# Optimization experiments

Measured on AMD Instinct MI355X. Metric: run time of the kernel, lower is better.

Reference implementation:

```python
import jax, jax.numpy as jnp
import numpy as np

B, S, D = 2, 2048, 1024
DFF = 2048
E_FFN = 8
E_ZERO = 4
E_TOT = E_FFN + E_ZERO
TOP_K = 2


def setup_inputs() -> dict:
    key = jax.random.key(0)
    k1, k2, k3, k4 = jax.random.split(key, 4)
    x = jax.random.normal(k1, (B, S, D), dtype=jnp.float32)
    gate_w = jax.random.normal(k2, (E_TOT, D), dtype=jnp.float32) * (1.0 / np.sqrt(D))
    expert_bias = jnp.zeros((E_TOT,), dtype=jnp.float32)
    w1 = jax.random.normal(k3, (E_FFN, DFF, D), dtype=jnp.float32) * (1.0 / np.sqrt(D))
    w2 = jax.random.normal(k4, (E_FFN, D, DFF), dtype=jnp.float32) * (1.0 / np.sqrt(DFF))
    return {"x": x, "gate_w": gate_w, "expert_bias": expert_bias, "w1": w1, "w2": w2}


def reference(x, gate_w, expert_bias, w1, w2):
    # Router: logits over all (FFN + zero) experts, plus adaptive bias buffer.
    logits = jnp.einsum('btd,ed->bte', x, gate_w) + expert_bias  # [B,S,E_TOT]
    topk_logits, topk_idx = jax.lax.top_k(logits, TOP_K)          # [B,S,K]
    topk_w = jax.nn.softmax(topk_logits, axis=-1)                 # renorm over top-k
    # Dense per-token per-expert combine weight (each expert appears at most once in top-k).
    onehot = jax.nn.one_hot(topk_idx, E_TOT, dtype=x.dtype)       # [B,S,K,E_TOT]
    w = jnp.einsum('btk,btke->bte', topk_w, onehot)               # [B,S,E_TOT]
    w_ffn = w[..., :E_FFN]                                        # [B,S,E_FFN]
    w_zero = jnp.sum(w[..., E_FFN:], axis=-1)                     # [B,S] (zero experts = identity)
    # Dense grouped FFN over all experts (eval mode: dropout is identity).
    h = jax.nn.silu(jnp.einsum('btd,efd->btef', x, w1))           # [B,S,E,DFF]
    y = jnp.einsum('btef,edf->bted', h, w2)                       # [B,S,E,D]
    out = jnp.einsum('bte,bted->btd', w_ffn, y) + w_zero[..., None] * x
    return out
```

## Files before the change

kernel.cpp:

```cpp
#include <hip/hip_runtime.h>
#include <math.h>

#define NTOK   4096
#define DMODEL 1024
#define DFFN   2048
#define NEXP   8
#define ETOT   12
#define MAXA   8192
#define WL1MAX (MAXA / 128 + NEXP)
#define WL2MAX (MAXA / 128 + NEXP)

typedef short  bf16x8 __attribute__((ext_vector_type(8)));
typedef float  f32x4  __attribute__((ext_vector_type(4)));

__device__ __forceinline__ unsigned short f2bf(float f) {
  unsigned int u = __float_as_uint(f);
  unsigned int r = (u + 0x7fffu + ((u >> 16) & 1u)) >> 16;
  return (unsigned short)r;
}

#define G2L16(g, l)                                                        \
  __builtin_amdgcn_global_load_lds(                                        \
      (const __attribute__((address_space(1))) void*)(g),                  \
      (__attribute__((address_space(3))) void*)(l), 16, 0, 0)

__global__ void cvt_kernel(const float* __restrict__ in,
                           unsigned short* __restrict__ outp, int n8) {
  int i = blockIdx.x * blockDim.x + threadIdx.x;
  if (i >= n8) return;
  const float4* p = (const float4*)in;
  float4 v0 = p[2 * (size_t)i], v1 = p[2 * (size_t)i + 1];
  ushort4 u0, u1;
  u0.x = f2bf(v0.x); u0.y = f2bf(v0.y); u0.z = f2bf(v0.z); u0.w = f2bf(v0.w);
  u1.x = f2bf(v1.x); u1.y = f2bf(v1.y); u1.z = f2bf(v1.z); u1.w = f2bf(v1.w);
  ((ushort4*)outp)[2 * (size_t)i]     = u0;
  ((ushort4*)outp)[2 * (size_t)i + 1] = u1;
}

__launch_bounds__(256)
__global__ void logits_kernel(const float* __restrict__ x,
                              const float* __restrict__ gw,
                              const float* __restrict__ eb,
                              float* __restrict__ logits) {
  __shared__ float gws[ETOT * DMODEL];
  int tid = threadIdx.x;
  const float4* gw4 = (const float4*)gw;
  float4* gws4 = (float4*)gws;
  #pragma unroll
  for (int i = 0; i < (ETOT * DMODEL / 4) / 256; i++)
    gws4[tid + i * 256] = gw4[tid + i * 256];
  __syncthreads();

  int sub = tid >> 4;
  int l16 = tid & 15;
  int tok = blockIdx.x * 16 + sub;
  const float4* xr = (const float4*)(x + (size_t)tok * DMODEL);

  float s[ETOT] = {};
  #pragma unroll
  for (int j = 0; j < 16; j++) {
    float4 xv = xr[l16 + j * 16];
    #pragma unroll
    for (int e = 0; e < ETOT; e++) {
      float4 g = gws4[e * (DMODEL / 4) + l16 + j * 16];
      s[e] += xv.x * g.x + xv.y * g.y + xv.z * g.z + xv.w * g.w;
    }
  }
  #pragma unroll
  for (int e = 0; e < ETOT; e++) {
    #pragma unroll
    for (int m = 8; m >= 1; m >>= 1) s[e] += __shfl_xor(s[e], m, 64);
  }
  if (l16 == 0) {
    #pragma unroll
    for (int e = 0; e < ETOT; e++)
      logits[(size_t)tok * ETOT + e] = s[e] + eb[e];
  }
}

__global__ void topk_kernel(const float* __restrict__ logits,
                            int* __restrict__ cnt,
                            int* __restrict__ choice,
                            float* __restrict__ chw,
                            float* __restrict__ wz) {
  int t = blockIdx.x * blockDim.x + threadIdx.x;
  if (t >= NTOK) return;
  const float4* lr = (const float4*)(logits + (size_t)t * ETOT);
  float4 a = lr[0], b = lr[1], c = lr[2];
  float lg[ETOT] = { a.x, a.y, a.z, a.w, b.x, b.y, b.z, b.w, c.x, c.y, c.z, c.w };
  int i1 = 0; float m1 = lg[0];
  #pragma unroll
  for (int e = 1; e < ETOT; e++) if (lg[e] > m1) { m1 = lg[e]; i1 = e; }
  int i2 = -1; float m2 = -3.4e38f;
  #pragma unroll
  for (int e = 0; e < ETOT; e++) { if (e == i1) continue; if (lg[e] > m2) { m2 = lg[e]; i2 = e; } }
  float ex = expf(m2 - m1);
  float w0 = 1.f / (1.f + ex);
  float w1 = ex / (1.f + ex);
  int ee[2] = { i1, i2 };
  float ww[2] = { w0, w1 };
  float z = 0.f;
  #pragma unroll
  for (int k = 0; k < 2; k++) {
    choice[t * 2 + k] = ee[k];
    chw[t * 2 + k]    = ww[k];
    if (ee[k] < NEXP) atomicAdd(&cnt[ee[k]], 1);
    else              z += ww[k];
  }
  wz[t] = z;
}

__global__ void scan_kernel(const int* __restrict__ cnt,
                            int* __restrict__ offs,
                            int* __restrict__ cursor,
                            int* __restrict__ wl1, int* __restrict__ nw1,
                            int* __restrict__ wl2, int* __restrict__ nw2) {
  if (threadIdx.x == 0) {
    int a = 0;
    for (int e = 0; e < NEXP; e++) { offs[e] = a; cursor[e] = a; a += cnt[e]; }
    int n1 = 0, n2 = 0;
    for (int e = 0; e < NEXP; e++) {
      int c = cnt[e];
      for (int mb = 0; mb * 128 < c; mb++) wl1[n1++] = e | (mb << 8);
      for (int mb = 0; mb * 128 < c; mb++) wl2[n2++] = e | (mb << 8);
    }
    *nw1 = n1; *nw2 = n2;
  }
}

__global__ void assign_kernel(const int* __restrict__ choice,
                              int* __restrict__ cursor,
                              int* __restrict__ a_row,
                              int* __restrict__ tok_list) {
  int t = blockIdx.x * blockDim.x + threadIdx.x;
  if (t >= NTOK) return;
  #pragma unroll
  for (int k = 0; k < 2; k++) {
    int e = choice[2 * t + k];
    if (e < NEXP) {
      int pos = atomicAdd(&cursor[e], 1);
      a_row[2 * t + k] = pos;
      tok_list[pos] = t;
    } else {
      a_row[2 * t + k] = -1;
    }
  }
}

template <int BM, int NDIM, int KDIM, bool SILU, bool AGATHER>
__launch_bounds__(256)
__global__ void ffn_gemm(const unsigned short* __restrict__ Abf,
                         const unsigned short* __restrict__ Bw,
                         const int* __restrict__ cnt,
                         const int* __restrict__ offs,
                         const int* __restrict__ tok_list,
                         const int* __restrict__ wl,
                         const int* __restrict__ nwork,
                         unsigned short* __restrict__ OutBf,
                         float* __restrict__ OutF) {
  constexpr int NB = NDIM / 128;
  constexpr int MI = BM / 32;
  constexpr int AJ = BM / 64;
  int id = blockIdx.x;
  int nb = id & (NB - 1);
  int wb = id / NB;
  if (wb >= *nwork) return;
  int w  = wl[wb];
  int e  = w & 255;
  int mb = w >> 8;
  int count = cnt[e];
  int m0 = mb * BM;
  int off = offs[e];
  int n0 = nb * 128;
  const unsigned short* B = Bw + (size_t)e * NDIM * KDIM;

  __shared__ unsigned short lA[2][BM * 32];
  __shared__ unsigned short lB[2][128 * 32];

  int tid  = threadIdx.x;
  int lane = tid & 63;
  int wv = tid >> 6;
  int wm = wv >> 1, wn = wv & 1;
  int lr = lane & 15, lk8 = (lane >> 4) * 8;

  int srow = tid >> 2;
  int scol = (tid & 3) * 8;
  const unsigned short* aSrc[AJ];
  const unsigned short* bSrc[2];
  #pragma unroll
  for (int j = 0; j < AJ; j++) {
    int rr = m0 + j * 64 + srow;
    if (rr >= count) rr = count - 1;
    if (AGATHER) aSrc[j] = Abf + (size_t)tok_list[off + rr] * KDIM + scol;
    else         aSrc[j] = Abf + (size_t)(off + rr) * KDIM + scol;
  }
  #pragma unroll
  for (int j = 0; j < 2; j++)
    bSrc[j] = B + (size_t)(n0 + j * 64 + srow) * KDIM + scol;

  f32x4 acc[MI][4] = {};

#define STAGE(b, kk)                                                        \
  do {                                                                      \
    int kb_ = (kk) * 32;                                                    \
    _Pragma("unroll")                                                       \
    for (int j = 0; j < AJ; j++) G2L16(aSrc[j] + kb_, &lA[b][j * 2048 + tid * 8]); \
    _Pragma("unroll")                                                       \
    for (int j = 0; j < 2; j++)  G2L16(bSrc[j] + kb_, &lB[b][j * 2048 + tid * 8]); \
  } while (0)

#define COMPUTE(b)                                                          \
  do {                                                                      \
    bf16x8 af[MI], bq[4];                                                   \
    _Pragma("unroll")                                                       \
    for (int mi = 0; mi < MI; mi++)                                         \
      af[mi] = *(const bf16x8*)&lA[b][(wm * (BM / 2) + mi * 16 + lr) * 32 + lk8]; \
    _Pragma("unroll")                                                       \
    for (int ni = 0; ni < 4; ni++)                                          \
      bq[ni] = *(const bf16x8*)&lB[b][(wn * 64 + ni * 16 + lr) * 32 + lk8]; \
    _Pragma("unroll")                                                       \
    for (int mi = 0; mi < MI; mi++)                                         \
      _Pragma("unroll")                                                     \
      for (int ni = 0; ni < 4; ni++)                                        \
        acc[mi][ni] = __builtin_amdgcn_mfma_f32_16x16x32_bf16(af[mi], bq[ni], acc[mi][ni], 0, 0, 0); \
  } while (0)

  constexpr int NK = KDIM / 32;
  STAGE(0, 0);
  __syncthreads();
  #pragma unroll 1
  for (int kk = 0; kk < NK; kk += 2) {
    if (kk + 1 < NK) STAGE(1, kk + 1);
    COMPUTE(0);
    __syncthreads();
    if (kk + 1 < NK) {
      if (kk + 2 < NK) STAGE(0, kk + 2);
      COMPUTE(1);
      __syncthreads();
    }
  }
#undef STAGE
#undef COMPUTE

  int rb = (lane >> 4) * 4;
  #pragma unroll
  for (int mi = 0; mi < MI; mi++) {
    #pragma unroll
    for (int i = 0; i < 4; i++) {
      int grow = m0 + wm * (BM / 2) + mi * 16 + rb + i;
      if (grow >= count) continue;
      #pragma unroll
      for (int ni = 0; ni < 4; ni++) {
        int gcol = n0 + wn * 64 + ni * 16 + lr;
        float v = acc[mi][ni][i];
        if (SILU) {
          float s = v * __builtin_amdgcn_rcpf(
                        1.f + __builtin_amdgcn_exp2f(-v * 1.44269504088896f));
          OutBf[(size_t)(off + grow) * NDIM + gcol] = f2bf(s);
        } else {
          OutF[(size_t)(off + grow) * NDIM + gcol] = v;
        }
      }
    }
  }
}

__global__ void combine_kernel(const float* __restrict__ x,
                               const float* __restrict__ Y,
                               const int* __restrict__ a_row,
                               const float* __restrict__ chw,
                               const float* __restrict__ wz,
                               float* __restrict__ out) {
  int t = blockIdx.x;
  int d = threadIdx.x * 4;
  const float4 xv = *(const float4*)&x[(size_t)t * DMODEL + d];
  float z = wz[t];
  float4 o; o.x = z * xv.x; o.y = z * xv.y; o.z = z * xv.z; o.w = z * xv.w;
  #pragma unroll
  for (int k = 0; k < 2; k++) {
    int r = a_row[2 * t + k];
    if (r >= 0) {
      float w = chw[2 * t + k];
      const float4 yv = *(const float4*)&Y[(size_t)r * DMODEL + d];
      o.x += w * yv.x; o.y += w * yv.y; o.z += w * yv.z; o.w += w * yv.w;
    }
  }
  *(float4*)&out[(size_t)t * DMODEL + d] = o;
}

extern "C" void kernel_launch(void* const* d_in, const int* in_sizes, int n_in,
                              void* d_out, int out_size, void* d_ws, size_t ws_size,
                              hipStream_t stream) {
  const float* x  = (const float*)d_in[0];
  const float* gw = (const float*)d_in[1];
  const float* eb = (const float*)d_in[2];
  const float* w1 = (const float*)d_in[3];
  const float* w2 = (const float*)d_in[4];
  float* out = (float*)d_out;

  char* ws = (char*)d_ws;
  size_t o = 0;
  int*   cnt     = (int*)(ws + o);  o += 8 * sizeof(int);
  int*   offs    = (int*)(ws + o);  o += 8 * sizeof(int);
  int*   cursor  = (int*)(ws + o);  o += 8 * sizeof(int);
  int*   nw1     = (int*)(ws + o);  o += sizeof(int);
  int*   nw2     = (int*)(ws + o);  o += sizeof(int);
  o = (o + 255) & ~(size_t)255;
  int*   wl1     = (int*)(ws + o);  o += WL1MAX * sizeof(int);
  int*   wl2     = (int*)(ws + o);  o += WL2MAX * sizeof(int);
  o = (o + 255) & ~(size_t)255;
  int*   choice  = (int*)(ws + o);  o += (size_t)2 * NTOK * sizeof(int);
  float* chw     = (float*)(ws + o); o += (size_t)2 * NTOK * sizeof(float);
  float* wzv     = (float*)(ws + o); o += (size_t)NTOK * sizeof(float);
  int*   a_row   = (int*)(ws + o);  o += (size_t)2 * NTOK * sizeof(int);
  int*   tok     = (int*)(ws + o);  o += (size_t)MAXA * sizeof(int);
  float* logits  = (float*)(ws + o); o += (size_t)NTOK * ETOT * sizeof(float);
  o = (o + 255) & ~(size_t)255;
  unsigned short* Xb  = (unsigned short*)(ws + o); o += (size_t)NTOK * DMODEL * sizeof(unsigned short);
  unsigned short* W1b = (unsigned short*)(ws + o); o += (size_t)NEXP * DFFN * DMODEL * sizeof(unsigned short);
  unsigned short* W2b = (unsigned short*)(ws + o); o += (size_t)NEXP * DMODEL * DFFN * sizeof(unsigned short);
  unsigned short* H   = (unsigned short*)(ws + o); o += (size_t)MAXA * DFFN * sizeof(unsigned short);
  float* Y = (float*)W1b;

  hipMemsetAsync(cnt, 0, 8 * sizeof(int), stream);

  cvt_kernel<<<dim3((NEXP * DFFN * DMODEL / 8 + 255) / 256), dim3(256), 0, stream>>>(
      w1, W1b, NEXP * DFFN * DMODEL / 8);
  cvt_kernel<<<dim3((NEXP * DMODEL * DFFN / 8 + 255) / 256), dim3(256), 0, stream>>>(
      w2, W2b, NEXP * DMODEL * DFFN / 8);
  cvt_kernel<<<dim3((NTOK * DMODEL / 8 + 255) / 256), dim3(256), 0, stream>>>(
      x, Xb, NTOK * DMODEL / 8);

  logits_kernel<<<dim3(NTOK / 16), dim3(256), 0, stream>>>(x, gw, eb, logits);
  topk_kernel<<<dim3(NTOK / 256), dim3(256), 0, stream>>>(logits, cnt, choice, chw, wzv);
  scan_kernel<<<dim3(1), dim3(64), 0, stream>>>(cnt, offs, cursor, wl1, nw1, wl2, nw2);
  assign_kernel<<<dim3(NTOK / 256), dim3(256), 0, stream>>>(choice, cursor, a_row, tok);

  ffn_gemm<128, DFFN, DMODEL, true, true>
      <<<dim3(WL1MAX * (DFFN / 128)), dim3(256), 0, stream>>>(
      Xb, W1b, cnt, offs, tok, wl1, nw1, H, nullptr);
  ffn_gemm<128, DMODEL, DFFN, false, false>
      <<<dim3(WL2MAX * (DMODEL / 128)), dim3(256), 0, stream>>>(
      H, W2b, cnt, offs, tok, wl2, nw2, nullptr, Y);

  combine_kernel<<<dim3(NTOK), dim3(256), 0, stream>>>(x, Y, a_row, chw, wzv, out);
}
```

Before: 197.7 us.

## Fuse fp32-to-bf16 weight conversion into grouped FFN GEMM B-tile loads

Removes the two standalone conversion kernels that turned w1 and w2 into bf16 workspace copies. The GEMMs now load fp32 weight tiles into registers, convert them to bf16 and write them to LDS, with the load overlapped against the MFMA compute of the other buffer. This avoids writing and re-reading roughly 64 MB of bf16 weights. In exchange each GEMM block reads twice the weight bytes in fp32, and the same weight tile is re-read and re-converted by every M-block of an expert. Y moves to its own workspace region because it can no longer alias W1b.

```diff
diff --git a/kernel.cpp b/kernel.cpp
--- a/kernel.cpp
+++ b/kernel.cpp
@@ -1,4 +1,5 @@
 #include <hip/hip_runtime.h>
+#include <hip/hip_bf16.h>
 #include <math.h>
 
 #define NTOK   4096
@@ -10,13 +11,19 @@
 #define WL1MAX (MAXA / 128 + NEXP)
 #define WL2MAX (MAXA / 128 + NEXP)
 
-typedef short  bf16x8 __attribute__((ext_vector_type(8)));
-typedef float  f32x4  __attribute__((ext_vector_type(4)));
+typedef short          bf16x8   __attribute__((ext_vector_type(8)));
+typedef float          f32x4    __attribute__((ext_vector_type(4)));
+typedef unsigned short ushort8v __attribute__((ext_vector_type(8)));
 
 __device__ __forceinline__ unsigned short f2bf(float f) {
   unsigned int u = __float_as_uint(f);
   unsigned int r = (u + 0x7fffu + ((u >> 16) & 1u)) >> 16;
   return (unsigned short)r;
+}
+
+__device__ __forceinline__ unsigned short f2bfh(float f) {
+  __hip_bfloat16 h = __float2bfloat16(f);
+  return __builtin_bit_cast(unsigned short, h);
 }
 
 #define G2L16(g, l)                                                        \
@@ -150,7 +157,7 @@
 template <int BM, int NDIM, int KDIM, bool SILU, bool AGATHER>
 __launch_bounds__(256)
 __global__ void ffn_gemm(const unsigned short* __restrict__ Abf,
-                         const unsigned short* __restrict__ Bw,
+                         const float* __restrict__ BwF,
                          const int* __restrict__ cnt,
                          const int* __restrict__ offs,
                          const int* __restrict__ tok_list,
@@ -172,7 +179,7 @@
   int m0 = mb * BM;
   int off = offs[e];
   int n0 = nb * 128;
-  const unsigned short* B = Bw + (size_t)e * NDIM * KDIM;
+  const float* B = BwF + (size_t)e * NDIM * KDIM;
 
   __shared__ unsigned short lA[2][BM * 32];
   __shared__ unsigned short lB[2][128 * 32];
@@ -186,7 +193,7 @@
   int srow = tid >> 2;
   int scol = (tid & 3) * 8;
   const unsigned short* aSrc[AJ];
-  const unsigned short* bSrc[2];
+  const float* bSrc[2];
   #pragma unroll
   for (int j = 0; j < AJ; j++) {
     int rr = m0 + j * 64 + srow;
@@ -199,14 +206,36 @@
     bSrc[j] = B + (size_t)(n0 + j * 64 + srow) * KDIM + scol;
 
   f32x4 acc[MI][4] = {};
-
-#define STAGE(b, kk)                                                        \
+  f32x4 breg[2][2];
+
+#define STAGEA(b, kk)                                                       \
   do {                                                                      \
     int kb_ = (kk) * 32;                                                    \
     _Pragma("unroll")                                                       \
     for (int j = 0; j < AJ; j++) G2L16(aSrc[j] + kb_, &lA[b][j * 2048 + tid * 8]); \
-    _Pragma("unroll")                                                       \
-    for (int j = 0; j < 2; j++)  G2L16(bSrc[j] + kb_, &lB[b][j * 2048 + tid * 8]); \
+  } while (0)
+
+#define LOADB(kk)                                                           \
+  do {                                                                      \
+    int kb_ = (kk) * 32;                                                    \
+    _Pragma("unroll")                                                       \
+    for (int j = 0; j < 2; j++) {                                           \
+      const f32x4* p_ = (const f32x4*)(bSrc[j] + kb_);                      \
+      breg[j][0] = p_[0]; breg[j][1] = p_[1];                               \
+    }                                                                       \
+  } while (0)
+
+#define WRITEB(b)                                                           \
+  do {                                                                      \
+    _Pragma("unroll")                                                       \
+    for (int j = 0; j < 2; j++) {                                           \
+      ushort8v u_;                                                          \
+      u_[0] = f2bfh(breg[j][0][0]); u_[1] = f2bfh(breg[j][0][1]);           \
+      u_[2] = f2bfh(breg[j][0][2]); u_[3] = f2bfh(breg[j][0][3]);           \
+      u_[4] = f2bfh(breg[j][1][0]); u_[5] = f2bfh(breg[j][1][1]);           \
+      u_[6] = f2bfh(breg[j][1][2]); u_[7] = f2bfh(breg[j][1][3]);           \
+      *(ushort8v*)&lB[b][j * 2048 + tid * 8] = u_;                          \
+    }                                                                       \
   } while (0)
 
 #define COMPUTE(b)                                                          \
@@ -226,20 +255,26 @@
   } while (0)
 
   constexpr int NK = KDIM / 32;
-  STAGE(0, 0);
+  LOADB(0);
+  STAGEA(0, 0);
+  WRITEB(0);
   __syncthreads();
   #pragma unroll 1
   for (int kk = 0; kk < NK; kk += 2) {
-    if (kk + 1 < NK) STAGE(1, kk + 1);
+    if (kk + 1 < NK) { LOADB(kk + 1); STAGEA(1, kk + 1); }
     COMPUTE(0);
+    if (kk + 1 < NK) WRITEB(1);
     __syncthreads();
     if (kk + 1 < NK) {
-      if (kk + 2 < NK) STAGE(0, kk + 2);
+      if (kk + 2 < NK) { LOADB(kk + 2); STAGEA(0, kk + 2); }
       COMPUTE(1);
+      if (kk + 2 < NK) WRITEB(0);
       __syncthreads();
     }
   }
-#undef STAGE
+#undef STAGEA
+#undef LOADB
+#undef WRITEB
 #undef COMPUTE
 
   int rb = (lane >> 4) * 4;
@@ -316,18 +351,12 @@
   int*   tok     = (int*)(ws + o);  o += (size_t)MAXA * sizeof(int);
   float* logits  = (float*)(ws + o); o += (size_t)NTOK * ETOT * sizeof(float);
   o = (o + 255) & ~(size_t)255;
-  unsigned short* Xb  = (unsigned short*)(ws + o); o += (size_t)NTOK * DMODEL * sizeof(unsigned short);
-  unsigned short* W1b = (unsigned short*)(ws + o); o += (size_t)NEXP * DFFN * DMODEL * sizeof(unsigned short);
-  unsigned short* W2b = (unsigned short*)(ws + o); o += (size_t)NEXP * DMODEL * DFFN * sizeof(unsigned short);
-  unsigned short* H   = (unsigned short*)(ws + o); o += (size_t)MAXA * DFFN * sizeof(unsigned short);
-  float* Y = (float*)W1b;
+  unsigned short* Xb = (unsigned short*)(ws + o); o += (size_t)NTOK * DMODEL * sizeof(unsigned short);
+  unsigned short* H  = (unsigned short*)(ws + o); o += (size_t)MAXA * DFFN * sizeof(unsigned short);
+  float*          Y  = (float*)(ws + o);          o += (size_t)MAXA * DMODEL * sizeof(float);
 
   hipMemsetAsync(cnt, 0, 8 * sizeof(int), stream);
 
-  cvt_kernel<<<dim3((NEXP * DFFN * DMODEL / 8 + 255) / 256), dim3(256), 0, stream>>>(
-      w1, W1b, NEXP * DFFN * DMODEL / 8);
-  cvt_kernel<<<dim3((NEXP * DMODEL * DFFN / 8 + 255) / 256), dim3(256), 0, stream>>>(
-      w2, W2b, NEXP * DMODEL * DFFN / 8);
   cvt_kernel<<<dim3((NTOK * DMODEL / 8 + 255) / 256), dim3(256), 0, stream>>>(
       x, Xb, NTOK * DMODEL / 8);
 
@@ -338,10 +367,10 @@
 
   ffn_gemm<128, DFFN, DMODEL, true, true>
       <<<dim3(WL1MAX * (DFFN / 128)), dim3(256), 0, stream>>>(
-      Xb, W1b, cnt, offs, tok, wl1, nw1, H, nullptr);
+      Xb, w1, cnt, offs, tok, wl1, nw1, H, nullptr);
   ffn_gemm<128, DMODEL, DFFN, false, false>
       <<<dim3(WL2MAX * (DMODEL / 128)), dim3(256), 0, stream>>>(
-      H, W2b, cnt, offs, tok, wl2, nw2, nullptr, Y);
+      H, w2, cnt, offs, tok, wl2, nw2, nullptr, Y);
 
   combine_kernel<<<dim3(NTOK), dim3(256), 0, stream>>>(x, Y, a_row, chw, wzv, out);
 }
```

Result: faster. 186.7 us (-5.6%).

## Fuse fp32-to-bf16 weight conversion into grouped FFN GEMM tile loads

Applied to the files above, without the earlier changes.

Drops the standalone conversion passes over w1 and w2 and instead streams fp32 weight tiles directly into LDS (with an XOR swizzle), converting to bf16 when building MFMA fragments. This removes a full read/write pass over both weight tensors per call. In exchange each GEMM reads twice as many weight bytes per tile, doubles B-tile LDS usage, and repeats conversion ALU work for every M-block that touches the same weights. Y gets its own workspace buffer since the bf16 weight buffer no longer exists.

```diff
diff --git a/kernel.cpp b/kernel.cpp
--- a/kernel.cpp
+++ b/kernel.cpp
@@ -1,4 +1,5 @@
 #include <hip/hip_runtime.h>
+#include <hip/hip_bf16.h>
 #include <math.h>
 
 #define NTOK   4096
@@ -10,13 +11,19 @@
 #define WL1MAX (MAXA / 128 + NEXP)
 #define WL2MAX (MAXA / 128 + NEXP)
 
-typedef short  bf16x8 __attribute__((ext_vector_type(8)));
-typedef float  f32x4  __attribute__((ext_vector_type(4)));
+typedef short          bf16x8   __attribute__((ext_vector_type(8)));
+typedef float          f32x4    __attribute__((ext_vector_type(4)));
+typedef unsigned short ushort8v __attribute__((ext_vector_type(8)));
 
 __device__ __forceinline__ unsigned short f2bf(float f) {
   unsigned int u = __float_as_uint(f);
   unsigned int r = (u + 0x7fffu + ((u >> 16) & 1u)) >> 16;
   return (unsigned short)r;
+}
+
+__device__ __forceinline__ unsigned short f2bfh(float f) {
+  __hip_bfloat16 h = __float2bfloat16(f);
+  return __builtin_bit_cast(unsigned short, h);
 }
 
 #define G2L16(g, l)                                                        \
@@ -150,7 +157,7 @@
 template <int BM, int NDIM, int KDIM, bool SILU, bool AGATHER>
 __launch_bounds__(256)
 __global__ void ffn_gemm(const unsigned short* __restrict__ Abf,
-                         const unsigned short* __restrict__ Bw,
+                         const float* __restrict__ BwF,
                          const int* __restrict__ cnt,
                          const int* __restrict__ offs,
                          const int* __restrict__ tok_list,
@@ -172,10 +179,10 @@
   int m0 = mb * BM;
   int off = offs[e];
   int n0 = nb * 128;
-  const unsigned short* B = Bw + (size_t)e * NDIM * KDIM;
+  const float* B = BwF + (size_t)e * NDIM * KDIM;
 
   __shared__ unsigned short lA[2][BM * 32];
-  __shared__ unsigned short lB[2][128 * 32];
+  __shared__ float          lBf[2][128 * 32];
 
   int tid  = threadIdx.x;
   int lane = tid & 63;
@@ -186,7 +193,6 @@
   int srow = tid >> 2;
   int scol = (tid & 3) * 8;
   const unsigned short* aSrc[AJ];
-  const unsigned short* bSrc[2];
   #pragma unroll
   for (int j = 0; j < AJ; j++) {
     int rr = m0 + j * 64 + srow;
@@ -194,9 +200,13 @@
     if (AGATHER) aSrc[j] = Abf + (size_t)tok_list[off + rr] * KDIM + scol;
     else         aSrc[j] = Abf + (size_t)(off + rr) * KDIM + scol;
   }
-  #pragma unroll
-  for (int j = 0; j < 2; j++)
-    bSrc[j] = B + (size_t)(n0 + j * 64 + srow) * KDIM + scol;
+  const float* bSrc[4];
+  #pragma unroll
+  for (int j = 0; j < 4; j++) {
+    int rr = j * 32 + (tid >> 3);
+    int c  = (tid & 7) ^ (rr & 7);
+    bSrc[j] = B + (size_t)(n0 + rr) * KDIM + c * 4;
+  }
 
   f32x4 acc[MI][4] = {};
 
@@ -206,7 +216,7 @@
     _Pragma("unroll")                                                       \
     for (int j = 0; j < AJ; j++) G2L16(aSrc[j] + kb_, &lA[b][j * 2048 + tid * 8]); \
     _Pragma("unroll")                                                       \
-    for (int j = 0; j < 2; j++)  G2L16(bSrc[j] + kb_, &lB[b][j * 2048 + tid * 8]); \
+    for (int j = 0; j < 4; j++)  G2L16(bSrc[j] + kb_, &lBf[b][j * 1024 + tid * 4]); \
   } while (0)
 
 #define COMPUTE(b)                                                          \
@@ -216,8 +226,20 @@
     for (int mi = 0; mi < MI; mi++)                                         \
       af[mi] = *(const bf16x8*)&lA[b][(wm * (BM / 2) + mi * 16 + lr) * 32 + lk8]; \
     _Pragma("unroll")                                                       \
-    for (int ni = 0; ni < 4; ni++)                                          \
-      bq[ni] = *(const bf16x8*)&lB[b][(wn * 64 + ni * 16 + lr) * 32 + lk8]; \
+    for (int ni = 0; ni < 4; ni++) {                                        \
+      int r_ = wn * 64 + ni * 16 + lr;                                      \
+      int sw_ = r_ & 7;                                                     \
+      int g0_ = (lk8 >> 2) ^ sw_;                                           \
+      int g1_ = ((lk8 >> 2) + 1) ^ sw_;                                     \
+      f32x4 t0 = *(const f32x4*)&lBf[b][r_ * 32 + g0_ * 4];                 \
+      f32x4 t1 = *(const f32x4*)&lBf[b][r_ * 32 + g1_ * 4];                 \
+      ushort8v u_;                                                          \
+      u_[0] = f2bfh(t0[0]); u_[1] = f2bfh(t0[1]);                           \
+      u_[2] = f2bfh(t0[2]); u_[3] = f2bfh(t0[3]);                           \
+      u_[4] = f2bfh(t1[0]); u_[5] = f2bfh(t1[1]);                           \
+      u_[6] = f2bfh(t1[2]); u_[7] = f2bfh(t1[3]);                           \
+      bq[ni] = __builtin_bit_cast(bf16x8, u_);                              \
+    }                                                                       \
     _Pragma("unroll")                                                       \
     for (int mi = 0; mi < MI; mi++)                                         \
       _Pragma("unroll")                                                     \
@@ -316,18 +338,12 @@
   int*   tok     = (int*)(ws + o);  o += (size_t)MAXA * sizeof(int);
   float* logits  = (float*)(ws + o); o += (size_t)NTOK * ETOT * sizeof(float);
   o = (o + 255) & ~(size_t)255;
-  unsigned short* Xb  = (unsigned short*)(ws + o); o += (size_t)NTOK * DMODEL * sizeof(unsigned short);
-  unsigned short* W1b = (unsigned short*)(ws + o); o += (size_t)NEXP * DFFN * DMODEL * sizeof(unsigned short);
-  unsigned short* W2b = (unsigned short*)(ws + o); o += (size_t)NEXP * DMODEL * DFFN * sizeof(unsigned short);
-  unsigned short* H   = (unsigned short*)(ws + o); o += (size_t)MAXA * DFFN * sizeof(unsigned short);
-  float* Y = (float*)W1b;
+  unsigned short* Xb = (unsigned short*)(ws + o); o += (size_t)NTOK * DMODEL * sizeof(unsigned short);
+  unsigned short* H  = (unsigned short*)(ws + o); o += (size_t)MAXA * DFFN * sizeof(unsigned short);
+  float*          Y  = (float*)(ws + o);          o += (size_t)MAXA * DMODEL * sizeof(float);
 
   hipMemsetAsync(cnt, 0, 8 * sizeof(int), stream);
 
-  cvt_kernel<<<dim3((NEXP * DFFN * DMODEL / 8 + 255) / 256), dim3(256), 0, stream>>>(
-      w1, W1b, NEXP * DFFN * DMODEL / 8);
-  cvt_kernel<<<dim3((NEXP * DMODEL * DFFN / 8 + 255) / 256), dim3(256), 0, stream>>>(
-      w2, W2b, NEXP * DMODEL * DFFN / 8);
   cvt_kernel<<<dim3((NTOK * DMODEL / 8 + 255) / 256), dim3(256), 0, stream>>>(
       x, Xb, NTOK * DMODEL / 8);
 
@@ -338,10 +354,10 @@
 
   ffn_gemm<128, DFFN, DMODEL, true, true>
       <<<dim3(WL1MAX * (DFFN / 128)), dim3(256), 0, stream>>>(
-      Xb, W1b, cnt, offs, tok, wl1, nw1, H, nullptr);
+      Xb, w1, cnt, offs, tok, wl1, nw1, H, nullptr);
   ffn_gemm<128, DMODEL, DFFN, false, false>
       <<<dim3(WL2MAX * (DMODEL / 128)), dim3(256), 0, stream>>>(
-      H, W2b, cnt, offs, tok, wl2, nw2, nullptr, Y);
+      H, w2, cnt, offs, tok, wl2, nw2, nullptr, Y);
 
   combine_kernel<<<dim3(NTOK), dim3(256), 0, stream>>>(x, Y, a_row, chw, wzv, out);
 }
```

After: 187.0 us. 5.5% less time.
